# Kernel tuning notes

Hardware: AMD Instinct MI355X
Metric: run time of the kernel (lower is better)

## Reference

```python
import jax, jax.numpy as jnp
import numpy as np

B, F, E, A = 2048, 64, 32, 4  # batch, features, embedding, attention_factor

def setup_inputs() -> dict:
    key = jax.random.key(0)
    k = jax.random.split(key, 6)
    return {
        "x": jax.random.normal(k[0], (B, F, E), dtype=jnp.float32),
        "attn_w": jax.random.normal(k[1], (E, A), dtype=jnp.float32) * (1.0 / np.sqrt(E)),
        "attn_b": jnp.zeros((A,), dtype=jnp.float32),
        "attn_h": jax.random.normal(k[2], (A, 1), dtype=jnp.float32) * (1.0 / np.sqrt(A)),
        "pool_w": jax.random.normal(k[3], (E, 1), dtype=jnp.float32) * (1.0 / np.sqrt(E)),
        "pool_b": jnp.zeros((1,), dtype=jnp.float32),
    }

def reference(x, attn_w, attn_b, attn_h, pool_w, pool_b):
    Fdim = x.shape[1]
    iu, ju = np.triu_indices(Fdim, k=1)  # pair indices i<j, P = F*(F-1)/2
    # pairwise element-wise products: [B, P, E]
    pairs = x[:, iu, :] * x[:, ju, :]
    # attention MLP: relu(pairs @ W + b) @ h -> [B, P, 1]
    dense = jax.nn.relu(jnp.einsum('bpe,ea->bpa', pairs, attn_w) + attn_b)
    scores = jnp.einsum('bpa,ao->bpo', dense, attn_h)
    attn = jax.nn.softmax(scores, axis=1)  # softmax over pair axis
    # softmax-weighted sum pooling over pairs -> [B, E]
    reduced = jnp.sum(attn * pairs, axis=1)
    # final dense to scalar (dropout is identity at inference)
    return reduced @ pool_w + pool_b  # [B, 1]
```

## Files before the change

### kernel.cpp

```cpp
#include <hip/hip_runtime.h>

typedef _Float16 f16x8 __attribute__((ext_vector_type(8)));
typedef _Float16 f16x4 __attribute__((ext_vector_type(4)));
typedef float    f32x4 __attribute__((ext_vector_type(4)));

#define FDIM 64
#define EDIM 32
#define ADIM 4
#define XH_S 56
#define XT_S 72
#define P_S  72

__global__ __launch_bounds__(256, 4)
void afm_kernel(const float* __restrict__ x,
                const float* __restrict__ attn_w,
                const float* __restrict__ attn_b,
                const float* __restrict__ attn_h,
                const float* __restrict__ pool_w,
                const float* __restrict__ pool_b,
                float* __restrict__ out)
{
    __shared__ _Float16 Xh[FDIM * XH_S];
    __shared__ _Float16 Xt[EDIM * XT_S];
    __shared__ _Float16 Pm[FDIM * P_S];
    __shared__ _Float16 Wh[ADIM * 32];
    __shared__ float ldsmax[4];
    __shared__ float ldssum[4];
    __shared__ float redw[4][EDIM];

    const int tid  = threadIdx.x;
    const int bb   = blockIdx.x;
    const int wave = tid >> 6;
    const int lane = tid & 63;
    const int n16  = lane & 15;
    const int q    = lane >> 4;

    const float* xb = x + (size_t)bb * (FDIM * EDIM);
    #pragma unroll
    for (int rep = 0; rep < 2; ++rep) {
        int idx4 = tid + rep * 256;
        int row  = idx4 >> 3;
        int c4   = idx4 & 7;
        float4 v = ((const float4*)xb)[idx4];
        _Float16 h0 = (_Float16)v.x, h1 = (_Float16)v.y,
                 h2 = (_Float16)v.z, h3 = (_Float16)v.w;
        f16x4 hv = {h0, h1, h2, h3};
        *(f16x4*)&Xh[row * XH_S + c4 * 4] = hv;
        int e0 = c4 * 4;
        Xt[(e0 + 0) * XT_S + row] = h0;
        Xt[(e0 + 1) * XT_S + row] = h1;
        Xt[(e0 + 2) * XT_S + row] = h2;
        Xt[(e0 + 3) * XT_S + row] = h3;
    }
    if (tid < ADIM * EDIM) {
        int a = tid & 3, e = tid >> 2;
        Wh[a * 32 + e] = (_Float16)attn_w[e * ADIM + a];
    }
    float hb[ADIM], hh[ADIM];
    #pragma unroll
    for (int a = 0; a < ADIM; ++a) { hb[a] = attn_b[a]; hh[a] = attn_h[a]; }
    __syncthreads();

    const int iA = wave * 16 + n16;
    f16x8 xafrag = *(const f16x8*)&Xh[iA * XH_S + q * 8];
    f16x8 bfrag[4];
    #pragma unroll
    for (int ct = 0; ct < 4; ++ct)
        bfrag[ct] = *(const f16x8*)&Xh[(ct * 16 + n16) * XH_S + q * 8];

    float s[4][4];
    #pragma unroll
    for (int ct = 0; ct < 4; ++ct)
        #pragma unroll
        for (int r = 0; r < 4; ++r) s[ct][r] = 0.f;

    #pragma unroll
    for (int a = 0; a < ADIM; ++a) {
        f16x8 wfrag = *(const f16x8*)&Wh[a * 32 + q * 8];
        f16x8 ya = xafrag * wfrag;
        #pragma unroll
        for (int ct = 0; ct < 4; ++ct) {
            f32x4 z = {0.f, 0.f, 0.f, 0.f};
            f32x4 acc = __builtin_amdgcn_mfma_f32_16x16x32_f16(ya, bfrag[ct], z, 0, 0, 0);
            #pragma unroll
            for (int r = 0; r < 4; ++r)
                s[ct][r] += fmaxf(acc[r] + hb[a], 0.f) * hh[a];
        }
    }

    float mloc = -1e30f;
    #pragma unroll
    for (int ct = 0; ct < 4; ++ct)
        #pragma unroll
        for (int r = 0; r < 4; ++r) {
            int i = wave * 16 + q * 4 + r;
            int j = ct * 16 + n16;
            if (i < j) mloc = fmaxf(mloc, s[ct][r]);
        }
    #pragma unroll
    for (int off = 32; off >= 1; off >>= 1)
        mloc = fmaxf(mloc, __shfl_xor(mloc, off));
    if (lane == 0) ldsmax[wave] = mloc;
    __syncthreads();
    float M = fmaxf(fmaxf(ldsmax[0], ldsmax[1]), fmaxf(ldsmax[2], ldsmax[3]));

    float psum = 0.f;
    #pragma unroll
    for (int ct = 0; ct < 4; ++ct)
        #pragma unroll
        for (int r = 0; r < 4; ++r) {
            int i = wave * 16 + q * 4 + r;
            int j = ct * 16 + n16;
            float p = (i < j) ? __expf(s[ct][r] - M) : 0.f;
            psum += p;
            Pm[i * P_S + j] = (_Float16)p;
        }
    #pragma unroll
    for (int off = 32; off >= 1; off >>= 1)
        psum += __shfl_xor(psum, off);
    if (lane == 0) ldssum[wave] = psum;
    __syncthreads();

    f16x8 pa0 = *(const f16x8*)&Pm[(wave * 16 + n16) * P_S + q * 8];
    f16x8 pa1 = *(const f16x8*)&Pm[(wave * 16 + n16) * P_S + 32 + q * 8];
    float tv[2];
    #pragma unroll
    for (int ctE = 0; ctE < 2; ++ctE) {
        f16x8 b0 = *(const f16x8*)&Xt[(ctE * 16 + n16) * XT_S + q * 8];
        f16x8 b1 = *(const f16x8*)&Xt[(ctE * 16 + n16) * XT_S + 32 + q * 8];
        f32x4 z = {0.f, 0.f, 0.f, 0.f};
        f32x4 acc = __builtin_amdgcn_mfma_f32_16x16x32_f16(pa0, b0, z, 0, 0, 0);
        acc = __builtin_amdgcn_mfma_f32_16x16x32_f16(pa1, b1, acc, 0, 0, 0);
        float t = 0.f;
        #pragma unroll
        for (int r = 0; r < 4; ++r) {
            int i = wave * 16 + q * 4 + r;
            int e = ctE * 16 + n16;
            t += acc[r] * (float)Xh[i * XH_S + e];
        }
        t += __shfl_xor(t, 16);
        t += __shfl_xor(t, 32);
        tv[ctE] = t;
    }
    if (q == 0) {
        redw[wave][n16]      = tv[0];
        redw[wave][16 + n16] = tv[1];
    }
    __syncthreads();

    if (tid < EDIM) {
        float S = ldssum[0] + ldssum[1] + ldssum[2] + ldssum[3];
        float v = (redw[0][tid] + redw[1][tid] + redw[2][tid] + redw[3][tid]) * pool_w[tid];
        #pragma unroll
        for (int off = 16; off >= 1; off >>= 1)
            v += __shfl_xor(v, off);
        if (tid == 0) out[bb] = v / S + pool_b[0];
    }
}

extern "C" void kernel_launch(void* const* d_in, const int* in_sizes, int n_in,
                              void* d_out, int out_size, void* d_ws, size_t ws_size,
                              hipStream_t stream) {
    const float* x      = (const float*)d_in[0];
    const float* attn_w = (const float*)d_in[1];
    const float* attn_b = (const float*)d_in[2];
    const float* attn_h = (const float*)d_in[3];
    const float* pool_w = (const float*)d_in[4];
    const float* pool_b = (const float*)d_in[5];
    float* out = (float*)d_out;
    int B = in_sizes[0] / (FDIM * EDIM);
    afm_kernel<<<B, 256, 0, stream>>>(x, attn_w, attn_b, attn_h, pool_w, pool_b, out);
}
```

Measured before the change: 76.89 us.

## Map one batch per wave, skip lower-triangle tiles, fold pool_w into MFMA

Each wave now handles a whole batch row, so the block-level syncs and the cross-wave reductions of max and sum go away. Only the 10 upper-triangular 16x16 pair tiles are computed instead of 16. The final pooling is restructured algebraically: pool_w is multiplied into x first, so each pair's projected value comes from one MFMA and is dotted with the softmax weights. That removes the P matrix, the transposed X, and the second GEMM. In exchange there are more registers per thread (launch bounds drop to 3 blocks), the grid shrinks to B/4 blocks, and pool_w is rounded to fp16, which adds some precision loss.

```diff
diff --git a/kernel.cpp b/kernel.cpp
--- a/kernel.cpp
+++ b/kernel.cpp
@@ -7,11 +7,11 @@
 #define FDIM 64
 #define EDIM 32
 #define ADIM 4
-#define XH_S 56
-#define XT_S 72
-#define P_S  72
+#define XH_S 40
 
-__global__ __launch_bounds__(256, 4)
+__device__ __constant__ int TBASE_host_unused[4] = {0, 4, 7, 9};
+
+__global__ __launch_bounds__(256, 3)
 void afm_kernel(const float* __restrict__ x,
                 const float* __restrict__ attn_w,
                 const float* __restrict__ attn_b,
@@ -20,142 +20,128 @@
                 const float* __restrict__ pool_b,
                 float* __restrict__ out)
 {
-    __shared__ _Float16 Xh[FDIM * XH_S];
-    __shared__ _Float16 Xt[EDIM * XT_S];
-    __shared__ _Float16 Pm[FDIM * P_S];
-    __shared__ _Float16 Wh[ADIM * 32];
-    __shared__ float ldsmax[4];
-    __shared__ float ldssum[4];
-    __shared__ float redw[4][EDIM];
+    __shared__ _Float16 Xh[4][FDIM * XH_S];
+    __shared__ _Float16 Wh[ADIM * EDIM];
+    __shared__ _Float16 Pwh[EDIM];
 
     const int tid  = threadIdx.x;
-    const int bb   = blockIdx.x;
     const int wave = tid >> 6;
     const int lane = tid & 63;
     const int n16  = lane & 15;
     const int q    = lane >> 4;
 
-    const float* xb = x + (size_t)bb * (FDIM * EDIM);
+    const int batch = blockIdx.x * 4 + wave;
+    const float* xb = x + (size_t)batch * (FDIM * EDIM);
+    _Float16* xh = Xh[wave];
+
     #pragma unroll
-    for (int rep = 0; rep < 2; ++rep) {
-        int idx4 = tid + rep * 256;
-        int row  = idx4 >> 3;
-        int c4   = idx4 & 7;
-        float4 v = ((const float4*)xb)[idx4];
-        _Float16 h0 = (_Float16)v.x, h1 = (_Float16)v.y,
-                 h2 = (_Float16)v.z, h3 = (_Float16)v.w;
-        f16x4 hv = {h0, h1, h2, h3};
-        *(f16x4*)&Xh[row * XH_S + c4 * 4] = hv;
-        int e0 = c4 * 4;
-        Xt[(e0 + 0) * XT_S + row] = h0;
-        Xt[(e0 + 1) * XT_S + row] = h1;
-        Xt[(e0 + 2) * XT_S + row] = h2;
-        Xt[(e0 + 3) * XT_S + row] = h3;
+    for (int k = 0; k < 8; ++k) {
+        int idx = lane + 64 * k;
+        float4 v = ((const float4*)xb)[idx];
+        int row = idx >> 3, c4 = idx & 7;
+        f16x4 hv = {(_Float16)v.x, (_Float16)v.y, (_Float16)v.z, (_Float16)v.w};
+        *(f16x4*)&xh[row * XH_S + c4 * 4] = hv;
     }
     if (tid < ADIM * EDIM) {
-        int a = tid & 3, e = tid >> 2;
-        Wh[a * 32 + e] = (_Float16)attn_w[e * ADIM + a];
+        int a = tid >> 5, e = tid & 31;
+        Wh[a * EDIM + e] = (_Float16)attn_w[e * ADIM + a];
+    } else if (tid < ADIM * EDIM + EDIM) {
+        int e = tid - ADIM * EDIM;
+        Pwh[e] = (_Float16)pool_w[e];
     }
     float hb[ADIM], hh[ADIM];
     #pragma unroll
     for (int a = 0; a < ADIM; ++a) { hb[a] = attn_b[a]; hh[a] = attn_h[a]; }
     __syncthreads();
 
-    const int iA = wave * 16 + n16;
-    f16x8 xafrag = *(const f16x8*)&Xh[iA * XH_S + q * 8];
-    f16x8 bfrag[4];
+    f16x8 bfrag[4], wfrag[4];
     #pragma unroll
     for (int ct = 0; ct < 4; ++ct)
-        bfrag[ct] = *(const f16x8*)&Xh[(ct * 16 + n16) * XH_S + q * 8];
+        bfrag[ct] = *(const f16x8*)&xh[(ct * 16 + n16) * XH_S + q * 8];
+    #pragma unroll
+    for (int a = 0; a < ADIM; ++a)
+        wfrag[a] = *(const f16x8*)&Wh[a * EDIM + q * 8];
+    f16x8 pwf = *(const f16x8*)&Pwh[q * 8];
 
-    float s[4][4];
+    float val[10][4];
     #pragma unroll
-    for (int ct = 0; ct < 4; ++ct)
+    for (int t = 0; t < 10; ++t)
         #pragma unroll
-        for (int r = 0; r < 4; ++r) s[ct][r] = 0.f;
+        for (int r = 0; r < 4; ++r) val[t][r] = 0.f;
 
+    const int tbase[4] = {0, 4, 7, 9};
     #pragma unroll
-    for (int a = 0; a < ADIM; ++a) {
-        f16x8 wfrag = *(const f16x8*)&Wh[a * 32 + q * 8];
-        f16x8 ya = xafrag * wfrag;
+    for (int mt = 0; mt < 4; ++mt) {
+        f16x8 xa = *(const f16x8*)&xh[(mt * 16 + n16) * XH_S + q * 8];
         #pragma unroll
-        for (int ct = 0; ct < 4; ++ct) {
-            f32x4 z = {0.f, 0.f, 0.f, 0.f};
-            f32x4 acc = __builtin_amdgcn_mfma_f32_16x16x32_f16(ya, bfrag[ct], z, 0, 0, 0);
+        for (int a = 0; a < ADIM; ++a) {
+            f16x8 ya = xa * wfrag[a];
             #pragma unroll
-            for (int r = 0; r < 4; ++r)
-                s[ct][r] += fmaxf(acc[r] + hb[a], 0.f) * hh[a];
+            for (int nt = mt; nt < 4; ++nt) {
+                f32x4 z = {0.f, 0.f, 0.f, 0.f};
+                f32x4 acc = __builtin_amdgcn_mfma_f32_16x16x32_f16(ya, bfrag[nt], z, 0, 0, 0);
+                int t = tbase[mt] + (nt - mt);
+                #pragma unroll
+                for (int r = 0; r < 4; ++r)
+                    val[t][r] += fmaxf(acc[r] + hb[a], 0.f) * hh[a];
+            }
         }
     }
 
-    float mloc = -1e30f;
+    float M = -3e38f;
     #pragma unroll
-    for (int ct = 0; ct < 4; ++ct)
+    for (int mt = 0; mt < 4; ++mt)
         #pragma unroll
-        for (int r = 0; r < 4; ++r) {
-            int i = wave * 16 + q * 4 + r;
-            int j = ct * 16 + n16;
-            if (i < j) mloc = fmaxf(mloc, s[ct][r]);
+        for (int nt = mt; nt < 4; ++nt) {
+            int t = tbase[mt] + (nt - mt);
+            #pragma unroll
+            for (int r = 0; r < 4; ++r) {
+                bool valid = (nt > mt) || ((q * 4 + r) < n16);
+                if (valid) M = fmaxf(M, val[t][r]);
+            }
         }
     #pragma unroll
     for (int off = 32; off >= 1; off >>= 1)
-        mloc = fmaxf(mloc, __shfl_xor(mloc, off));
-    if (lane == 0) ldsmax[wave] = mloc;
-    __syncthreads();
-    float M = fmaxf(fmaxf(ldsmax[0], ldsmax[1]), fmaxf(ldsmax[2], ldsmax[3]));
+        M = fmaxf(M, __shfl_xor(M, off));
 
     float psum = 0.f;
     #pragma unroll
-    for (int ct = 0; ct < 4; ++ct)
+    for (int mt = 0; mt < 4; ++mt)
         #pragma unroll
-        for (int r = 0; r < 4; ++r) {
-            int i = wave * 16 + q * 4 + r;
-            int j = ct * 16 + n16;
-            float p = (i < j) ? __expf(s[ct][r] - M) : 0.f;
-            psum += p;
-            Pm[i * P_S + j] = (_Float16)p;
+        for (int nt = mt; nt < 4; ++nt) {
+            int t = tbase[mt] + (nt - mt);
+            #pragma unroll
+            for (int r = 0; r < 4; ++r) {
+                bool valid = (nt > mt) || ((q * 4 + r) < n16);
+                float p = valid ? __expf(val[t][r] - M) : 0.f;
+                val[t][r] = p;
+                psum += p;
+            }
         }
+
+    float dot = 0.f;
     #pragma unroll
-    for (int off = 32; off >= 1; off >>= 1)
+    for (int mt = 0; mt < 4; ++mt) {
+        f16x8 xa = *(const f16x8*)&xh[(mt * 16 + n16) * XH_S + q * 8];
+        f16x8 yp = xa * pwf;
+        #pragma unroll
+        for (int nt = mt; nt < 4; ++nt) {
+            f32x4 z = {0.f, 0.f, 0.f, 0.f};
+            f32x4 g = __builtin_amdgcn_mfma_f32_16x16x32_f16(yp, bfrag[nt], z, 0, 0, 0);
+            int t = tbase[mt] + (nt - mt);
+            #pragma unroll
+            for (int r = 0; r < 4; ++r)
+                dot += val[t][r] * g[r];
+        }
+    }
+
+    #pragma unroll
+    for (int off = 32; off >= 1; off >>= 1) {
+        dot  += __shfl_xor(dot, off);
         psum += __shfl_xor(psum, off);
-    if (lane == 0) ldssum[wave] = psum;
-    __syncthreads();
-
-    f16x8 pa0 = *(const f16x8*)&Pm[(wave * 16 + n16) * P_S + q * 8];
-    f16x8 pa1 = *(const f16x8*)&Pm[(wave * 16 + n16) * P_S + 32 + q * 8];
-    float tv[2];
-    #pragma unroll
-    for (int ctE = 0; ctE < 2; ++ctE) {
-        f16x8 b0 = *(const f16x8*)&Xt[(ctE * 16 + n16) * XT_S + q * 8];
-        f16x8 b1 = *(const f16x8*)&Xt[(ctE * 16 + n16) * XT_S + 32 + q * 8];
-        f32x4 z = {0.f, 0.f, 0.f, 0.f};
-        f32x4 acc = __builtin_amdgcn_mfma_f32_16x16x32_f16(pa0, b0, z, 0, 0, 0);
-        acc = __builtin_amdgcn_mfma_f32_16x16x32_f16(pa1, b1, acc, 0, 0, 0);
-        float t = 0.f;
-        #pragma unroll
-        for (int r = 0; r < 4; ++r) {
-            int i = wave * 16 + q * 4 + r;
-            int e = ctE * 16 + n16;
-            t += acc[r] * (float)Xh[i * XH_S + e];
-        }
-        t += __shfl_xor(t, 16);
-        t += __shfl_xor(t, 32);
-        tv[ctE] = t;
     }
-    if (q == 0) {
-        redw[wave][n16]      = tv[0];
-        redw[wave][16 + n16] = tv[1];
-    }
-    __syncthreads();
-
-    if (tid < EDIM) {
-        float S = ldssum[0] + ldssum[1] + ldssum[2] + ldssum[3];
-        float v = (redw[0][tid] + redw[1][tid] + redw[2][tid] + redw[3][tid]) * pool_w[tid];
-        #pragma unroll
-        for (int off = 16; off >= 1; off >>= 1)
-            v += __shfl_xor(v, off);
-        if (tid == 0) out[bb] = v / S + pool_b[0];
-    }
+    if (lane == 0)
+        out[batch] = dot / psum + pool_b[0];
 }
 
 extern "C" void kernel_launch(void* const* d_in, const int* in_sizes, int n_in,
@@ -169,5 +155,5 @@
     const float* pool_b = (const float*)d_in[5];
     float* out = (float*)d_out;
     int B = in_sizes[0] / (FDIM * EDIM);
-    afm_kernel<<<B, 256, 0, stream>>>(x, attn_w, attn_b, attn_h, pool_w, pool_b, out);
+    afm_kernel<<<B / 4, 256, 0, stream>>>(x, attn_w, attn_b, attn_h, pool_w, pool_b, out);
 }
```

Result: no change. 76.28 us (-0.8%).
